# Performance work log

Measured on AMD Instinct MI355X. Metric: run time of the kernel, lower is better.

## Reference

```python
import jax, jax.numpy as jnp
import numpy as np

# Module constants (from Flanger.__init__ defaults and forward defaults)
SAMPLE_RATE = 44100
BASE_DELAY_MS = 5.0
DELAY_RANGE_MS = 4.0
RATE = 0.5      # LFO rate (Hz)
DEPTH = 0.7     # modulation depth
FEEDBACK = 0.3  # feedback amount (clamped to 0.9 in forward)
MIX = 0.5       # dry/wet mix


def _next_pow2(n):
    p = 1
    while p < n:
        p *= 2
    return p


def _delay_schedule(T):
    """Host-side precompute of the data-independent delay schedule.
    Matches the torch loop: int() truncation, & mask circular wrap."""
    base = int(BASE_DELAY_MS * SAMPLE_RATE / 1000)               # 220
    rng = int(DELAY_RANGE_MS * SAMPLE_RATE / 1000 * DEPTH)       # 123
    max_delay = int((BASE_DELAY_MS + DELAY_RANGE_MS) * SAMPLE_RATE / 1000) + 10
    buf_size = _next_pow2(max_delay)                             # 512
    mask = buf_size - 1
    t = np.arange(T, dtype=np.float64)
    phase = (t * RATE / SAMPLE_RATE) % 1.0
    mod = np.sin(2.0 * np.pi * phase)
    delay = base + np.trunc(mod * rng).astype(np.int64)          # int() truncates toward zero
    delay = np.clip(delay, 1, buf_size - 1)
    write_idx = (np.arange(T, dtype=np.int64) & mask)
    read_idx = (write_idx - delay) & mask
    return buf_size, read_idx.astype(np.int32), write_idx.astype(np.int32)


def setup_inputs() -> dict:
    key = jax.random.key(0)
    x = jax.random.normal(key, (64, 220500), dtype=jnp.float32)  # [B, T] = 64 clips of 5s @ 44.1kHz
    return {"x": x}


def reference(x):
    B, T = x.shape
    buf_size, read_idx, write_idx = _delay_schedule(T)
    fb = min(FEEDBACK, 0.9)

    def step(buffer, inp):
        xt, ri, wi = inp                       # xt: [B], ri/wi: scalar int32
        delayed = buffer[:, ri]                # [B] circular-buffer read
        out_t = xt * (1.0 - MIX) + delayed * MIX
        buffer = buffer.at[:, wi].set(xt + delayed * fb)  # feedback write
        return buffer, out_t

    buffer0 = jnp.zeros((B, buf_size), dtype=x.dtype)
    xs = (x.T, jnp.asarray(read_idx), jnp.asarray(write_idx))
    _, out = jax.lax.scan(step, buffer0, xs)   # out: [T, B]
    return out.T
```

## Files before the change

kernel.cpp:

```cpp
#include <hip/hip_runtime.h>
#include <math.h>

#define T_LEN 220500
#define FB 0.3f
#define KMAX 4
#define TPB 1792
#define NI 7
#define TILE_BACK 1376
#define TILE_USED (TPB + TILE_BACK)
#define TILE_PAD 3200
#define BPB 2
#define NTH 256

typedef float f2 __attribute__((ext_vector_type(2)));

__device__ __forceinline__ int delay_at(int cur) {
    double phase = fmod(((double)cur * 0.5) / 44100.0, 1.0);
    double mod = sin(2.0 * M_PI * phase);
    int delay = 220 + (int)trunc(mod * 123.0);
    if (delay < 1) delay = 1;
    if (delay > 511) delay = 511;
    return delay;
}

__global__ void expand_kernel(unsigned short* __restrict__ Dw, int T, int TT) {
    int t = blockIdx.x * NTH + threadIdx.x;
    if (t >= TT) return;
    int tb  = t / TPB;
    int r   = t - tb * TPB;
    int i   = r >> 8;
    int tid = r & 255;
    unsigned short* base = Dw + (((size_t)tb * KMAX) * 256 + tid) * 8 + i;
    int cur = t;
    int cum4 = 0;
    bool live = (t < T);
    #pragma unroll
    for (int k = 0; k < KMAX; ++k) {
        int inc = 97;
        if (live) {
            inc = delay_at(cur);
            cur -= inc;
            if (cur < 0) live = false;
        }
        cum4 += inc << 2;
        base[(size_t)k * (256 * 8)] = (unsigned short)cum4;
    }
}

__global__ __launch_bounds__(NTH) void gather_kernel(
    const float* __restrict__ x, const unsigned short* __restrict__ Dw,
    float* __restrict__ out, int T, int B) {
    const int b0  = blockIdx.x * BPB;
    const int tb  = blockIdx.y;
    const int tid = threadIdx.x;
    const int t0  = tb * TPB;
    const bool has2 = (b0 + 1 < B);
    __shared__ float tile[2 * TILE_PAD];

    const unsigned short* __restrict__ db =
        Dw + (((size_t)tb * KMAX) * 256 + tid) * 8;
    uint4 w0 = *(const uint4*)(db);
    uint4 w1 = *(const uint4*)(db + 256 * 8);
    uint4 w2 = *(const uint4*)(db + 2 * 256 * 8);
    uint4 w3 = *(const uint4*)(db + 3 * 256 * 8);

    const int g0 = t0 - TILE_BACK;
    const bool interior = (g0 >= 0) && (g0 + TILE_USED <= T);
    const float* __restrict__ xb0 = x + (size_t)b0 * T;
    const float* __restrict__ xb1 = xb0 + (has2 ? T : 0);

    if (interior) {
        #pragma unroll
        for (int s = 0; s < 4; ++s) {
            int j4 = (s * NTH + tid) * 4;
            if (j4 < TILE_USED) {
                __builtin_amdgcn_global_load_lds(
                    (const __attribute__((address_space(1))) void*)(xb0 + g0 + j4),
                    (__attribute__((address_space(3))) void*)(tile + j4), 16, 0, 0);
                __builtin_amdgcn_global_load_lds(
                    (const __attribute__((address_space(1))) void*)(xb1 + g0 + j4),
                    (__attribute__((address_space(3))) void*)(tile + TILE_PAD + j4), 16, 0, 0);
            }
        }
    } else {
        for (int bb = 0; bb < BPB; ++bb) {
            const float* __restrict__ xb = (bb == 0) ? xb0 : xb1;
            #pragma unroll
            for (int s = 0; s < 4; ++s) {
                int j4 = (s * NTH + tid) * 4;
                if (j4 < TILE_USED) {
                    int g = g0 + j4;
                    float4 v;
                    if (g >= 0 && g <= T - 4) {
                        v = *(const float4*)(xb + g);
                    } else {
                        v.x = (g     >= 0 && g     < T) ? xb[g]     : 0.0f;
                        v.y = (g + 1 >= 0 && g + 1 < T) ? xb[g + 1] : 0.0f;
                        v.z = (g + 2 >= 0 && g + 2 < T) ? xb[g + 2] : 0.0f;
                        v.w = (g + 3 >= 0 && g + 3 < T) ? xb[g + 3] : 0.0f;
                    }
                    *(float4*)(tile + bb * TILE_PAD + j4) = v;
                }
            }
        }
    }
    __syncthreads();

    const char* __restrict__ tb8 = (const char*)tile;

    int ab[NI];
    f2  acc[NI];
    #pragma unroll
    for (int i = 0; i < NI; ++i) {
        ab[i] = (TILE_BACK + tid + 256 * i) * 4;
        f2 v;
        v.x = *(const float*)(tb8 + ab[i]);
        v.y = *(const float*)(tb8 + ab[i] + TILE_PAD * 4);
        acc[i] = 0.5f * v;
    }

    float coef = 0.5f;
    #pragma unroll
    for (int k = 0; k < KMAX; ++k) {
        uint4 w = (k == 0) ? w0 : (k == 1) ? w1 : (k == 2) ? w2 : w3;
        f2 cc; cc.x = coef; cc.y = coef;
        #pragma unroll
        for (int i = 0; i < NI; ++i) {
            unsigned wj = (i < 2) ? w.x : (i < 4) ? w.y : (i < 6) ? w.z : w.w;
            int c4 = (i & 1) ? (int)(wj >> 16) : (int)(wj & 0xFFFFu);
            int a = ab[i] - c4;
            f2 v;
            v.x = *(const float*)(tb8 + a);
            v.y = *(const float*)(tb8 + a + TILE_PAD * 4);
            acc[i] += cc * v;
        }
        coef *= FB;
    }

    float* __restrict__ ob0 = out + (size_t)b0 * T;
    float* __restrict__ ob1 = out + (size_t)(has2 ? b0 + 1 : b0) * T;
    if (t0 + TPB <= T) {
        #pragma unroll
        for (int i = 0; i < NI; ++i) {
            int t = t0 + tid + 256 * i;
            ob0[t] = acc[i].x;
            if (has2) ob1[t] = acc[i].y;
        }
    } else {
        #pragma unroll
        for (int i = 0; i < NI; ++i) {
            int t = t0 + tid + 256 * i;
            if (t < T) {
                ob0[t] = acc[i].x;
                if (has2) ob1[t] = acc[i].y;
            }
        }
    }
}

__global__ __launch_bounds__(256) void flanger_direct_kernel(
    const float* __restrict__ x, float* __restrict__ out, int T) {
    int t = blockIdx.x * blockDim.x + threadIdx.x;
    if (t >= T) return;
    int b = blockIdx.y;
    const float* xb = x + (size_t)b * T;
    float acc = 0.5f * xb[t];
    float coef = 0.5f;
    int cur = t;
    #pragma unroll 1
    for (int k = 0; k < 8; ++k) {
        cur -= delay_at(cur);
        if (cur < 0) break;
        acc += coef * xb[cur];
        coef *= FB;
    }
    out[(size_t)b * T + t] = acc;
}

extern "C" void kernel_launch(void* const* d_in, const int* in_sizes, int n_in,
                              void* d_out, int out_size, void* d_ws, size_t ws_size,
                              hipStream_t stream) {
    const float* x = (const float*)d_in[0];
    float* out = (float*)d_out;
    const int T = T_LEN;
    const int B = in_sizes[0] / T;

    const int TB = (T + TPB - 1) / TPB;
    const int TT = TB * TPB;

    unsigned short* Dw = (unsigned short*)d_ws;
    size_t need = (size_t)TB * KMAX * 256 * 8 * sizeof(unsigned short);

    if (ws_size >= need) {
        expand_kernel<<<(TT + NTH - 1) / NTH, NTH, 0, stream>>>(Dw, T, TT);
        dim3 grid((B + BPB - 1) / BPB, TB);
        gather_kernel<<<grid, NTH, 0, stream>>>(x, Dw, out, T, B);
    } else {
        dim3 grid((T + 255) / 256, B);
        flanger_direct_kernel<<<grid, 256, 0, stream>>>(x, out, T);
    }
}
```

Baseline: 32.93 us.

## Shrink gather tile to 1024 samples with paired outputs and vector stores

Cuts the per-block time span from 1792 to 1024 samples, so each thread now handles two adjacent sample pairs and writes float2 stores. The delay-offset table is repacked so each thread reads two uint4 words instead of four, and those loads are issued after the tile copy is started. Launch bounds ask for 8 blocks per SM. The 1376-sample look-back halo stays the same while the tile shrinks, so the redundant halo load grows relative to useful work, traded against more blocks and higher occupancy.

```diff
diff --git a/kernel.cpp b/kernel.cpp
--- a/kernel.cpp
+++ b/kernel.cpp
@@ -4,11 +4,10 @@
 #define T_LEN 220500
 #define FB 0.3f
 #define KMAX 4
-#define TPB 1792
-#define NI 7
+#define TPB 1024
 #define TILE_BACK 1376
 #define TILE_USED (TPB + TILE_BACK)
-#define TILE_PAD 3200
+#define TILE_PAD 2432
 #define BPB 2
 #define NTH 256
 
@@ -26,11 +25,12 @@
 __global__ void expand_kernel(unsigned short* __restrict__ Dw, int T, int TT) {
     int t = blockIdx.x * NTH + threadIdx.x;
     if (t >= TT) return;
-    int tb  = t / TPB;
-    int r   = t - tb * TPB;
-    int i   = r >> 8;
-    int tid = r & 255;
-    unsigned short* base = Dw + (((size_t)tb * KMAX) * 256 + tid) * 8 + i;
+    int tb  = t >> 10;
+    int r   = t & 1023;
+    int i   = r >> 9;
+    int e   = r & 1;
+    int tid = (r >> 1) & 255;
+    unsigned short* base = Dw + (((size_t)tb * 2) * 256 + tid) * 8 + i * 2 + e;
     int cur = t;
     int cum4 = 0;
     bool live = (t < T);
@@ -43,11 +43,11 @@
             if (cur < 0) live = false;
         }
         cum4 += inc << 2;
-        base[(size_t)k * (256 * 8)] = (unsigned short)cum4;
-    }
-}
-
-__global__ __launch_bounds__(NTH) void gather_kernel(
+        base[(size_t)(k >> 1) * (256 * 8) + (k & 1) * 4] = (unsigned short)cum4;
+    }
+}
+
+__global__ __launch_bounds__(NTH, 8) void gather_kernel(
     const float* __restrict__ x, const unsigned short* __restrict__ Dw,
     float* __restrict__ out, int T, int B) {
     const int b0  = blockIdx.x * BPB;
@@ -57,13 +57,6 @@
     const bool has2 = (b0 + 1 < B);
     __shared__ float tile[2 * TILE_PAD];
 
-    const unsigned short* __restrict__ db =
-        Dw + (((size_t)tb * KMAX) * 256 + tid) * 8;
-    uint4 w0 = *(const uint4*)(db);
-    uint4 w1 = *(const uint4*)(db + 256 * 8);
-    uint4 w2 = *(const uint4*)(db + 2 * 256 * 8);
-    uint4 w3 = *(const uint4*)(db + 3 * 256 * 8);
-
     const int g0 = t0 - TILE_BACK;
     const bool interior = (g0 >= 0) && (g0 + TILE_USED <= T);
     const float* __restrict__ xb0 = x + (size_t)b0 * T;
@@ -71,7 +64,7 @@
 
     if (interior) {
         #pragma unroll
-        for (int s = 0; s < 4; ++s) {
+        for (int s = 0; s < 3; ++s) {
             int j4 = (s * NTH + tid) * 4;
             if (j4 < TILE_USED) {
                 __builtin_amdgcn_global_load_lds(
@@ -86,7 +79,7 @@
         for (int bb = 0; bb < BPB; ++bb) {
             const float* __restrict__ xb = (bb == 0) ? xb0 : xb1;
             #pragma unroll
-            for (int s = 0; s < 4; ++s) {
+            for (int s = 0; s < 3; ++s) {
                 int j4 = (s * NTH + tid) * 4;
                 if (j4 < TILE_USED) {
                     int g = g0 + j4;
@@ -104,55 +97,64 @@
             }
         }
     }
+
+    const unsigned short* __restrict__ db =
+        Dw + (((size_t)tb * 2) * 256 + tid) * 8;
+    uint4 w0 = *(const uint4*)(db);
+    uint4 w1 = *(const uint4*)(db + 256 * 8);
+
     __syncthreads();
 
     const char* __restrict__ tb8 = (const char*)tile;
 
-    int ab[NI];
-    f2  acc[NI];
-    #pragma unroll
-    for (int i = 0; i < NI; ++i) {
-        ab[i] = (TILE_BACK + tid + 256 * i) * 4;
-        f2 v;
-        v.x = *(const float*)(tb8 + ab[i]);
-        v.y = *(const float*)(tb8 + ab[i] + TILE_PAD * 4);
-        acc[i] = 0.5f * v;
-    }
-
-    float coef = 0.5f;
-    #pragma unroll
-    for (int k = 0; k < KMAX; ++k) {
-        uint4 w = (k == 0) ? w0 : (k == 1) ? w1 : (k == 2) ? w2 : w3;
-        f2 cc; cc.x = coef; cc.y = coef;
+    int ab[2];
+    f2  acc[2][2];
+    #pragma unroll
+    for (int i = 0; i < 2; ++i) {
+        ab[i] = (TILE_BACK + 2 * tid + 512 * i) * 4;
         #pragma unroll
-        for (int i = 0; i < NI; ++i) {
-            unsigned wj = (i < 2) ? w.x : (i < 4) ? w.y : (i < 6) ? w.z : w.w;
-            int c4 = (i & 1) ? (int)(wj >> 16) : (int)(wj & 0xFFFFu);
-            int a = ab[i] - c4;
+        for (int e = 0; e < 2; ++e) {
+            int a = ab[i] + 4 * e;
             f2 v;
             v.x = *(const float*)(tb8 + a);
             v.y = *(const float*)(tb8 + a + TILE_PAD * 4);
-            acc[i] += cc * v;
+            acc[i][e] = 0.5f * v;
+        }
+    }
+
+    float coef = 0.5f;
+    #pragma unroll
+    for (int k = 0; k < KMAX; ++k) {
+        uint4 w = (k < 2) ? w0 : w1;
+        f2 cc; cc.x = coef; cc.y = coef;
+        #pragma unroll
+        for (int i = 0; i < 2; ++i) {
+            unsigned u = (k & 1) ? ((i == 0) ? w.z : w.w)
+                                 : ((i == 0) ? w.x : w.y);
+            #pragma unroll
+            for (int e = 0; e < 2; ++e) {
+                int c4 = (e == 0) ? (int)(u & 0xFFFFu) : (int)(u >> 16);
+                int a = ab[i] + 4 * e - c4;
+                f2 v;
+                v.x = *(const float*)(tb8 + a);
+                v.y = *(const float*)(tb8 + a + TILE_PAD * 4);
+                acc[i][e] += cc * v;
+            }
         }
         coef *= FB;
     }
 
     float* __restrict__ ob0 = out + (size_t)b0 * T;
     float* __restrict__ ob1 = out + (size_t)(has2 ? b0 + 1 : b0) * T;
-    if (t0 + TPB <= T) {
-        #pragma unroll
-        for (int i = 0; i < NI; ++i) {
-            int t = t0 + tid + 256 * i;
-            ob0[t] = acc[i].x;
-            if (has2) ob1[t] = acc[i].y;
-        }
-    } else {
-        #pragma unroll
-        for (int i = 0; i < NI; ++i) {
-            int t = t0 + tid + 256 * i;
-            if (t < T) {
-                ob0[t] = acc[i].x;
-                if (has2) ob1[t] = acc[i].y;
+    #pragma unroll
+    for (int i = 0; i < 2; ++i) {
+        int t = t0 + 2 * tid + 512 * i;
+        if (t < T) {
+            f2 s0; s0.x = acc[i][0].x; s0.y = acc[i][1].x;
+            *(f2*)(ob0 + t) = s0;
+            if (has2) {
+                f2 s1; s1.x = acc[i][0].y; s1.y = acc[i][1].y;
+                *(f2*)(ob1 + t) = s1;
             }
         }
     }
@@ -189,7 +191,7 @@
     const int TT = TB * TPB;
 
     unsigned short* Dw = (unsigned short*)d_ws;
-    size_t need = (size_t)TB * KMAX * 256 * 8 * sizeof(unsigned short);
+    size_t need = (size_t)TB * 2 * 256 * 8 * sizeof(unsigned short);
 
     if (ws_size >= need) {
         expand_kernel<<<(TT + NTH - 1) / NTH, NTH, 0, stream>>>(Dw, T, TT);
```

Result: faster. 31.66 us (-3.9%).
